# Kernel tuning notes

Measured on AMD Instinct MI355X. Metric: run time of the kernel, lower is better.

Reference implementation:

```python
import jax, jax.numpy as jnp
import numpy as np

N_NODES = 100000
N_EDGES = 1600000
IN_DIM, HID_DIM, OUT_DIM = 128, 128, 64


def setup_inputs() -> dict:
    key = jax.random.key(0)
    k1, k2, k3, k4 = jax.random.split(key, 4)
    x = jax.random.normal(k1, (N_NODES, IN_DIM), dtype=jnp.float32)
    edge_index = jax.random.randint(k2, (2, N_EDGES), 0, N_NODES, dtype=jnp.int64)
    # Glorot-ish init for weights, zeros for biases (as in PyG GCNConv defaults)
    W1 = jax.random.normal(k3, (IN_DIM, HID_DIM), dtype=jnp.float32) * (1.0 / np.sqrt(IN_DIM))
    b1 = jnp.zeros((HID_DIM,), dtype=jnp.float32)
    W2 = jax.random.normal(k4, (HID_DIM, OUT_DIM), dtype=jnp.float32) * (1.0 / np.sqrt(HID_DIM))
    b2 = jnp.zeros((OUT_DIM,), dtype=jnp.float32)
    return {"x": x, "edge_index": edge_index, "W1": W1, "b1": b1, "W2": W2, "b2": b2}


def _build_norm(edge_index, num_nodes):
    """Add self-loops and compute symmetric GCN normalization per edge.
    Returns (src, dst, norm) with self-loops appended."""
    loops = jnp.arange(num_nodes, dtype=edge_index.dtype)
    src = jnp.concatenate([edge_index[0], loops])
    dst = jnpp_concat = jnp.concatenate([edge_index[1], loops])
    deg = jax.ops.segment_sum(jnp.ones_like(dst, dtype=jnp.float32), dst,
                              num_segments=num_nodes)
    dinv = jax.lax.rsqrt(deg)  # deg >= 1 due to self-loops
    norm = dinv[src] * dinv[dst]  # [E + N]
    return src, dst, norm


def _gcn_conv(h, W, b, src, dst, norm, num_nodes):
    h = h @ W                                   # [N, F_out]
    msg = h[src] * norm[:, None]                # gather + scale, [E+N, F_out]
    agg = jax.ops.segment_sum(msg, dst, num_segments=num_nodes)
    return agg + b


def reference(x, edge_index, W1, b1, W2, b2):
    num_nodes = x.shape[0]
    src, dst, norm = _build_norm(edge_index, num_nodes)
    h = jax.nn.relu(_gcn_conv(x, W1, b1, src, dst, norm, num_nodes))
    return _gcn_conv(h, W2, b2, src, dst, norm, num_nodes)
```

## Files before the change

### kernel.cpp

```cpp
#include <hip/hip_runtime.h>

#define NN 100000
#define NE 1600000
#define NB 782
#define NBPAD 1024
#define CAPB 3072
#define EPB 8192
#define BFT 1024
#define NROWPAD 100096
#define DPAD 136
#define OPAD 72
#define MAXE 64

typedef __attribute__((ext_vector_type(8))) short short8;
typedef __attribute__((ext_vector_type(4))) float f32x4;

__device__ __forceinline__ unsigned short bf16rn(float f) {
    unsigned u = __float_as_uint(f);
    return (unsigned short)((u + 0x7FFFu + ((u >> 16) & 1u)) >> 16);
}
__device__ __forceinline__ float4 bf2x4(uint2 g) {
    float4 r;
    r.x = __uint_as_float(g.x << 16);
    r.y = __uint_as_float(g.x & 0xFFFF0000u);
    r.z = __uint_as_float(g.y << 16);
    r.w = __uint_as_float(g.y & 0xFFFF0000u);
    return r;
}
__device__ __forceinline__ uint2 packbf4(float4 v) {
    uint2 u;
    u.x = (unsigned)bf16rn(v.x) | ((unsigned)bf16rn(v.y) << 16);
    u.y = (unsigned)bf16rn(v.z) | ((unsigned)bf16rn(v.w) << 16);
    return u;
}
__device__ __forceinline__ void acc4(float4& a, uint2 v, float q) {
    a.x = fmaf(__uint_as_float(v.x << 16), q, a.x);
    a.y = fmaf(__uint_as_float(v.x & 0xFFFF0000u), q, a.y);
    a.z = fmaf(__uint_as_float(v.y << 16), q, a.z);
    a.w = fmaf(__uint_as_float(v.y & 0xFFFF0000u), q, a.w);
}
__device__ __forceinline__ float decq(unsigned e) {
    return __uint_as_float(0x38000000u | ((e & 0x7FFFu) << 12));
}
__device__ __forceinline__ int xcd_swz(int bid, int nwg) {
    int q = nwg >> 3, r = nwg & 7;
    int x = bid & 7, j = bid >> 3;
    int base = (x < r) ? x * (q + 1) : r * (q + 1) + (x - r) * q;
    return base + j;
}

__global__ void detect_i64_k(const unsigned* __restrict__ ei, int* __restrict__ flag) {
    unsigned w = ei[2 * threadIdx.x + 1];
    unsigned long long b = __ballot(w == 0u);
    if (threadIdx.x == 0) *flag = (b == 0xFFFFFFFFFFFFFFFFull) ? 1 : 0;
}
__device__ __forceinline__ int load_node(const void* ei, int i64, long long idx) {
    return i64 ? (int)((const long long*)ei)[idx] : ((const int*)ei)[idx];
}

__global__ void cast_bf16_k(const float* __restrict__ in, ushort* __restrict__ outb,
                            long long n4) {
    long long i = (long long)blockIdx.x * 256 + threadIdx.x;
    if (i >= n4) return;
    ((uint2*)outb)[i] = packbf4(((const float4*)in)[i]);
}

__global__ void prep_wt_k(const float* __restrict__ W1, const float* __restrict__ W2,
                          ushort* __restrict__ W1t, ushort* __restrict__ W2t) {
    int i = blockIdx.x * 256 + threadIdx.x;
    if (i < 128 * 128) {
        int k = i >> 7, n = i & 127;
        W1t[n * 128 + k] = bf16rn(W1[k * 128 + n]);
    }
    if (i < 128 * 64) {
        int k = i >> 6, n = i & 63;
        W2t[n * 128 + k] = bf16rn(W2[k * 64 + n]);
    }
}

__global__ __launch_bounds__(1024) void binfill_k(const void* __restrict__ ei,
                                                  const int* __restrict__ flag,
                                                  int* __restrict__ cur,
                                                  unsigned* __restrict__ bstage) {
    __shared__ unsigned binned[EPB];
    __shared__ int lcnt[NBPAD];
    __shared__ int lpos[NBPAD];
    __shared__ int gbase[NBPAD];
    __shared__ int tsum[NBPAD];
    int tid = threadIdx.x;
    long long e0 = (long long)blockIdx.x * EPB;
    int i64 = *flag;

    lcnt[tid] = 0;
    __syncthreads();

    for (int i = tid; i < EPB; i += BFT) {
        long long e = e0 + i;
        if (e < NE) {
            int d = load_node(ei, i64, (long long)NE + e);
            atomicAdd(&lcnt[d >> 7], 1);
        }
    }
    __syncthreads();

    int c = lcnt[tid];
    tsum[tid] = c;
    __syncthreads();
    for (int off = 1; off < NBPAD; off <<= 1) {
        int v = (tid >= off) ? tsum[tid - off] : 0;
        __syncthreads();
        tsum[tid] += v;
        __syncthreads();
    }
    int excl = tsum[tid] - c;
    lcnt[tid] = excl;
    lpos[tid] = excl;
    if (tid < NB) gbase[tid] = c ? atomicAdd(&cur[tid], c) : 0;
    __syncthreads();

    for (int i = tid; i < EPB; i += BFT) {
        long long e = e0 + i;
        if (e < NE) {
            int sv = load_node(ei, i64, e);
            int d  = load_node(ei, i64, (long long)NE + e);
            int b  = d >> 7;
            int p  = atomicAdd(&lpos[b], 1);
            binned[p] = ((unsigned)(d & 127) << 17) | (unsigned)sv;
        }
    }
    __syncthreads();

    if (tid < NB) {
        int start = lcnt[tid], endp = lpos[tid];
        int gb = gbase[tid];
        unsigned* dst = bstage + (long long)tid * CAPB;
        for (int k = start; k < endp; k++) {
            int go = gb + (k - start);
            if (go < CAPB) dst[go] = binned[k];
        }
    }
}

__global__ __launch_bounds__(256) void regroup_k(const int* __restrict__ cur,
                                                 const unsigned* __restrict__ bstage,
                                                 int* __restrict__ cnt,
                                                 int* __restrict__ rowstart,
                                                 unsigned* __restrict__ grouped,
                                                 float* __restrict__ dinv) {
    __shared__ unsigned stash[CAPB];
    __shared__ unsigned srt[CAPB];
    __shared__ int lcnt[128], lofs[128], lpos[128], sc[128];
    int tid = threadIdx.x;
    int b = blockIdx.x;

    int total = cur[b];
    if (total > CAPB) total = CAPB;
    const unsigned* seg = bstage + (long long)b * CAPB;
    for (int i = tid; i < total; i += 256) stash[i] = seg[i];
    __syncthreads();

    if (tid < 128) { lcnt[tid] = 0; lpos[tid] = 0; }
    __syncthreads();
    for (int i = tid; i < total; i += 256)
        atomicAdd(&lcnt[stash[i] >> 17], 1);
    __syncthreads();

    if (tid < 128) sc[tid] = lcnt[tid];
    __syncthreads();
    for (int off = 1; off < 128; off <<= 1) {
        int v = 0;
        if (tid < 128 && tid >= off) v = sc[tid - off];
        __syncthreads();
        if (tid < 128) sc[tid] += v;
        __syncthreads();
    }
    if (tid < 128) {
        lofs[tid] = sc[tid] - lcnt[tid];
        int node = b * 128 + tid;
        if (node < NN) {
            cnt[node] = lcnt[tid];
            rowstart[node] = b * CAPB + lofs[tid];
            dinv[node] = rsqrtf((float)(lcnt[tid] + 1));
        }
    }
    __syncthreads();

    for (int i = tid; i < total; i += 256) {
        unsigned e = stash[i];
        int nl = e >> 17;
        int p = atomicAdd(&lpos[nl], 1);
        srt[lofs[nl] + p] = e;
    }
    __syncthreads();

    unsigned* g = grouped + (long long)b * CAPB;
    for (int i = tid; i < total; i += 256) g[i] = srt[i] & 0x1FFFFu;
}

__global__ __launch_bounds__(256) void qn2_k(const int* __restrict__ cur,
                                             const float* __restrict__ dinv,
                                             unsigned* __restrict__ grouped) {
    int b = blockIdx.x;
    int total = cur[b];
    if (total > CAPB) total = CAPB;
    unsigned* g = grouped + (long long)b * CAPB;
    for (int i = threadIdx.x; i < total; i += 256) {
        unsigned s = g[i];
        unsigned bits = __float_as_uint(dinv[s]);
        g[i] = (s << 15) | ((bits >> 12) & 0x7FFFu);
    }
}

template <int LPN, bool BIAS, bool OUTB>
__global__ __launch_bounds__(256) void pull6_k(const unsigned* __restrict__ grouped,
                                               const int* __restrict__ rowstart,
                                               const int* __restrict__ cnt,
                                               const float* __restrict__ dinv,
                                               const ushort* __restrict__ hb,
                                               const float* __restrict__ bias,
                                               void* __restrict__ out) {
    __shared__ unsigned ed[256 / LPN][MAXE];
    int tid = threadIdx.x;
    int nib = tid / LPN;
    int lane = tid & (LPN - 1);
    int node = xcd_swz(blockIdx.x, (int)gridDim.x) * (256 / LPN) + nib;
    if (node >= NN) return;

    const uint2* h2 = (const uint2*)hb;
    float di = dinv[node];
    float w0 = di * di;
    float4 A = make_float4(0.f, 0.f, 0.f, 0.f);
    float4 B = make_float4(0.f, 0.f, 0.f, 0.f);
    {
        float4 hv = bf2x4(h2[(unsigned)node * LPN + lane]);
        A.x = hv.x * w0; A.y = hv.y * w0; A.z = hv.z * w0; A.w = hv.w * w0;
    }

    int deg = cnt[node];
    const unsigned* row = grouped + rowstart[node];
    int s = deg < MAXE ? deg : MAXE;

    for (int t = lane; t < s; t += LPN) ed[nib][t] = row[t];

    int j = 0;
    if (s >= 8) {
        uint2 v[8];
        float q[8];
#pragma unroll
        for (int t = 0; t < 8; t++) {
            unsigned e = ed[nib][t];
            q[t] = decq(e) * di;
            v[t] = h2[(e >> 15) * LPN + lane];
        }
        for (; j + 16 <= s; j += 8) {
#pragma unroll
            for (int t = 0; t < 8; t++) {
                unsigned e = ed[nib][j + 8 + t];
                uint2 nv = h2[(e >> 15) * LPN + lane];
                if (t & 1) acc4(B, v[t], q[t]);
                else       acc4(A, v[t], q[t]);
                v[t] = nv; q[t] = decq(e) * di;
            }
        }
#pragma unroll
        for (int t = 0; t < 8; t++) {
            if (t & 1) acc4(B, v[t], q[t]);
            else       acc4(A, v[t], q[t]);
        }
        j += 8;
    }
    for (; j < s; j++) {
        unsigned e = ed[nib][j];
        uint2 v0 = h2[(e >> 15) * LPN + lane];
        acc4(A, v0, decq(e) * di);
    }
    for (; j < deg; j++) {
        unsigned e = row[j];
        uint2 v0 = h2[(e >> 15) * LPN + lane];
        acc4(A, v0, decq(e) * di);
    }

    float4 o;
    o.x = A.x + B.x; o.y = A.y + B.y; o.z = A.z + B.z; o.w = A.w + B.w;
    if (BIAS) {
        float4 bb = ((const float4*)bias)[lane];
        o.x += bb.x; o.y += bb.y; o.z += bb.z; o.w += bb.w;
    }
    if (OUTB)
        ((uint2*)out)[(unsigned)node * LPN + lane] = packbf4(o);
    else
        ((float4*)out)[(unsigned)node * LPN + lane] = o;
}

__global__ __launch_bounds__(256) void dgemm_mfma_k(const ushort* __restrict__ Ab,
                                                    const ushort* __restrict__ W1t,
                                                    const float* __restrict__ b1,
                                                    const ushort* __restrict__ W2t,
                                                    ushort* __restrict__ H2b) {
    __shared__ ushort Tt[4][32 * DPAD];
    __shared__ ushort Ot[4][32 * OPAD];
    int tid = threadIdx.x;
    int wv = tid >> 6, lane = tid & 63;
    int m16 = lane & 15, quad = lane >> 4;
    int row0 = blockIdx.x * 128 + wv * 32;

    short8 af[2][4];
#pragma unroll
    for (int mt = 0; mt < 2; mt++)
#pragma unroll
        for (int kc = 0; kc < 4; kc++)
            af[mt][kc] = *(const short8*)(Ab + (long long)(row0 + mt * 16 + m16) * 128
                                          + kc * 32 + quad * 8);
    f32x4 accA[2][8];
#pragma unroll
    for (int mt = 0; mt < 2; mt++)
#pragma unroll
        for (int nt = 0; nt < 8; nt++) accA[mt][nt] = (f32x4){0.f, 0.f, 0.f, 0.f};

#pragma unroll
    for (int nt = 0; nt < 8; nt++) {
#pragma unroll
        for (int kc = 0; kc < 4; kc++) {
            short8 bf = *(const short8*)(W1t + (nt * 16 + m16) * 128 + kc * 32 + quad * 8);
            accA[0][nt] = __builtin_amdgcn_mfma_f32_16x16x32_bf16(af[0][kc], bf, accA[0][nt], 0, 0, 0);
            accA[1][nt] = __builtin_amdgcn_mfma_f32_16x16x32_bf16(af[1][kc], bf, accA[1][nt], 0, 0, 0);
        }
    }

#pragma unroll
    for (int nt = 0; nt < 8; nt++) {
        float bb = b1[nt * 16 + m16];
#pragma unroll
        for (int mt = 0; mt < 2; mt++)
#pragma unroll
            for (int r = 0; r < 4; r++) {
                float v = fmaxf(accA[mt][nt][r] + bb, 0.f);
                Tt[wv][(mt * 16 + quad * 4 + r) * DPAD + nt * 16 + m16] = bf16rn(v);
            }
    }
    __syncthreads();

    f32x4 accB[2][4];
#pragma unroll
    for (int mt = 0; mt < 2; mt++)
#pragma unroll
        for (int nt = 0; nt < 4; nt++) accB[mt][nt] = (f32x4){0.f, 0.f, 0.f, 0.f};

#pragma unroll
    for (int nt = 0; nt < 4; nt++) {
#pragma unroll
        for (int kc = 0; kc < 4; kc++) {
            short8 bf = *(const short8*)(W2t + (nt * 16 + m16) * 128 + kc * 32 + quad * 8);
#pragma unroll
            for (int mt = 0; mt < 2; mt++) {
                short8 aT = *(const short8*)(&Tt[wv][(mt * 16 + m16) * DPAD + kc * 32 + quad * 8]);
                accB[mt][nt] = __builtin_amdgcn_mfma_f32_16x16x32_bf16(aT, bf, accB[mt][nt], 0, 0, 0);
            }
        }
    }

#pragma unroll
    for (int nt = 0; nt < 4; nt++)
#pragma unroll
        for (int mt = 0; mt < 2; mt++)
#pragma unroll
            for (int r = 0; r < 4; r++)
                Ot[wv][(mt * 16 + quad * 4 + r) * OPAD + nt * 16 + m16] = bf16rn(accB[mt][nt][r]);
    __syncthreads();

    uint4* H4 = (uint4*)H2b;
#pragma unroll
    for (int it = 0; it < 4; it++) {
        int idx = it * 64 + lane;
        int r = idx >> 3, c = idx & 7;
        int grow = row0 + r;
        if (grow < NN) {
            uint4 v = *(const uint4*)(&Ot[wv][r * OPAD + c * 8]);
            H4[(long long)grow * 8 + c] = v;
        }
    }
}

extern "C" void kernel_launch(void* const* d_in, const int* in_sizes, int n_in,
                              void* d_out, int out_size, void* d_ws, size_t ws_size,
                              hipStream_t stream) {
    const float* x  = (const float*)d_in[0];
    const void*  ei = d_in[1];
    const float* W1 = (const float*)d_in[2];
    const float* b1 = (const float*)d_in[3];
    const float* W2 = (const float*)d_in[4];
    const float* b2 = (const float*)d_in[5];
    float* out = (float*)d_out;
    char* ws = (char*)d_ws;

    int*      flag     = (int*)ws;
    int*      cur      = (int*)(ws + 0x1000);
    int*      cnt      = (int*)(ws + 0x10000);
    int*      rowstart = (int*)(ws + 0x80000);
    unsigned* bstage   = (unsigned*)(ws + 0x100000);
    unsigned* grouped  = (unsigned*)(ws + 0xB00000);
    ushort*   xb       = (ushort*)(ws + 0x1500000);
    ushort*   aggxb    = (ushort*)(ws + 0x2F00000);
    ushort*   h2b      = (ushort*)(ws + 0x4800000);
    ushort*   W1t      = (ushort*)(ws + 0x5500000);
    ushort*   W2t      = (ushort*)(ws + 0x5510000);
    float*    dinv     = (float*)(ws + 0x5520000);

    hipMemsetAsync(cur, 0, NB * sizeof(int), stream);
    detect_i64_k<<<1, 64, 0, stream>>>((const unsigned*)ei, flag);
    cast_bf16_k<<<(NN * 32 + 255) / 256, 256, 0, stream>>>(x, xb, (long long)NN * 32);
    prep_wt_k<<<64, 256, 0, stream>>>(W1, W2, W1t, W2t);
    binfill_k<<<(NE + EPB - 1) / EPB, BFT, 0, stream>>>(ei, flag, cur, bstage);
    regroup_k<<<NB, 256, 0, stream>>>(cur, bstage, cnt, rowstart, grouped, dinv);
    qn2_k<<<NB, 256, 0, stream>>>(cur, dinv, grouped);

    pull6_k<32, false, true><<<(NN + 7) / 8, 256, 0, stream>>>(grouped, rowstart, cnt, dinv,
                                                               xb, nullptr, aggxb);
    dgemm_mfma_k<<<NROWPAD / 128, 256, 0, stream>>>(aggxb, W1t, b1, W2t, h2b);

    pull6_k<16, true, false><<<(NN + 15) / 16, 256, 0, stream>>>(grouped, rowstart, cnt, dinv,
                                                                 h2b, b2, out);
}
```

Before: 278.1 us.

## Split feature tables into column chunks and block-stage edge lists in LDS

The feature tables (bf16 x and layer-2 hidden) are re-laid out into column-chunk-major slabs of 16 features per node. Each pull block handles 64 nodes for a single chunk, with blockIdx low bits choosing the chunk. The intent is that the gathered working set per chunk is small enough to stay in L2/MALL cache. Each block stages the whole contiguous edge range of its 64 nodes into shared memory, replacing the per-node MAXE cap and tail path, and outputs use nontemporal stores. In exchange, the edge list is read NCH times, each gather is only 8 bytes, and a block's edge range larger than CAPB would overflow shared memory.

```diff
diff --git a/kernel.cpp b/kernel.cpp
--- a/kernel.cpp
+++ b/kernel.cpp
@@ -7,25 +7,18 @@
 #define CAPB 3072
 #define EPB 8192
 #define BFT 1024
+#define NPB 1563
 #define NROWPAD 100096
 #define DPAD 136
 #define OPAD 72
-#define MAXE 64
 
 typedef __attribute__((ext_vector_type(8))) short short8;
 typedef __attribute__((ext_vector_type(4))) float f32x4;
+typedef __attribute__((ext_vector_type(2))) unsigned u32x2;
 
 __device__ __forceinline__ unsigned short bf16rn(float f) {
     unsigned u = __float_as_uint(f);
     return (unsigned short)((u + 0x7FFFu + ((u >> 16) & 1u)) >> 16);
-}
-__device__ __forceinline__ float4 bf2x4(uint2 g) {
-    float4 r;
-    r.x = __uint_as_float(g.x << 16);
-    r.y = __uint_as_float(g.x & 0xFFFF0000u);
-    r.z = __uint_as_float(g.y << 16);
-    r.w = __uint_as_float(g.y & 0xFFFF0000u);
-    return r;
 }
 __device__ __forceinline__ uint2 packbf4(float4 v) {
     uint2 u;
@@ -42,12 +35,6 @@
 __device__ __forceinline__ float decq(unsigned e) {
     return __uint_as_float(0x38000000u | ((e & 0x7FFFu) << 12));
 }
-__device__ __forceinline__ int xcd_swz(int bid, int nwg) {
-    int q = nwg >> 3, r = nwg & 7;
-    int x = bid & 7, j = bid >> 3;
-    int base = (x < r) ? x * (q + 1) : r * (q + 1) + (x - r) * q;
-    return base + j;
-}
 
 __global__ void detect_i64_k(const unsigned* __restrict__ ei, int* __restrict__ flag) {
     unsigned w = ei[2 * threadIdx.x + 1];
@@ -58,11 +45,14 @@
     return i64 ? (int)((const long long*)ei)[idx] : ((const int*)ei)[idx];
 }
 
-__global__ void cast_bf16_k(const float* __restrict__ in, ushort* __restrict__ outb,
-                            long long n4) {
+__global__ void cast_xc_k(const float* __restrict__ in, ushort* __restrict__ xc) {
     long long i = (long long)blockIdx.x * 256 + threadIdx.x;
-    if (i >= n4) return;
-    ((uint2*)outb)[i] = packbf4(((const float4*)in)[i]);
+    if (i >= (long long)NN * 32) return;
+    int node = (int)(i >> 5);
+    int fq = (int)(i & 31);
+    int ch = fq >> 2, ln = fq & 3;
+    ((uint2*)xc)[(long long)ch * (NN * 4) + (long long)node * 4 + ln] =
+        packbf4(((const float4*)in)[i]);
 }
 
 __global__ void prep_wt_k(const float* __restrict__ W1, const float* __restrict__ W2,
@@ -211,52 +201,60 @@
     }
 }
 
-template <int LPN, bool BIAS, bool OUTB>
-__global__ __launch_bounds__(256) void pull6_k(const unsigned* __restrict__ grouped,
+template <int NCH, bool BIAS, bool OUTB>
+__global__ __launch_bounds__(256) void pull7_k(const unsigned* __restrict__ grouped,
                                                const int* __restrict__ rowstart,
                                                const int* __restrict__ cnt,
                                                const float* __restrict__ dinv,
-                                               const ushort* __restrict__ hb,
+                                               const ushort* __restrict__ tbl,
                                                const float* __restrict__ bias,
-                                               void* __restrict__ out) {
-    __shared__ unsigned ed[256 / LPN][MAXE];
+                                               void* __restrict__ outp) {
+    __shared__ unsigned eds[CAPB];
     int tid = threadIdx.x;
-    int nib = tid / LPN;
-    int lane = tid & (LPN - 1);
-    int node = xcd_swz(blockIdx.x, (int)gridDim.x) * (256 / LPN) + nib;
+    int bid = blockIdx.x;
+    int c  = bid & (NCH - 1);
+    int nb = bid / NCH;
+    int node0 = nb * 64;
+
+    int nlast = node0 + 63; if (nlast >= NN) nlast = NN - 1;
+    int base = rowstart[node0];
+    int size = rowstart[nlast] + cnt[nlast] - base;
+    for (int i = tid; i < size; i += 256)
+        eds[i] = __builtin_nontemporal_load(&grouped[base + i]);
+
+    int node = node0 + (tid >> 2);
+    int lane = tid & 3;
+    __syncthreads();
     if (node >= NN) return;
 
-    const uint2* h2 = (const uint2*)hb;
+    const uint2* tc = (const uint2*)tbl + (long long)c * (NN * 4);
     float di = dinv[node];
     float w0 = di * di;
     float4 A = make_float4(0.f, 0.f, 0.f, 0.f);
     float4 B = make_float4(0.f, 0.f, 0.f, 0.f);
     {
-        float4 hv = bf2x4(h2[(unsigned)node * LPN + lane]);
-        A.x = hv.x * w0; A.y = hv.y * w0; A.z = hv.z * w0; A.w = hv.w * w0;
+        uint2 sv = tc[(unsigned)node * 4 + lane];
+        acc4(A, sv, w0);
     }
 
     int deg = cnt[node];
-    const unsigned* row = grouped + rowstart[node];
-    int s = deg < MAXE ? deg : MAXE;
-
-    for (int t = lane; t < s; t += LPN) ed[nib][t] = row[t];
+    int off = rowstart[node] - base;
 
     int j = 0;
-    if (s >= 8) {
+    if (deg >= 8) {
         uint2 v[8];
         float q[8];
 #pragma unroll
         for (int t = 0; t < 8; t++) {
-            unsigned e = ed[nib][t];
+            unsigned e = eds[off + t];
             q[t] = decq(e) * di;
-            v[t] = h2[(e >> 15) * LPN + lane];
-        }
-        for (; j + 16 <= s; j += 8) {
+            v[t] = tc[(e >> 15) * 4 + lane];
+        }
+        for (; j + 16 <= deg; j += 8) {
 #pragma unroll
             for (int t = 0; t < 8; t++) {
-                unsigned e = ed[nib][j + 8 + t];
-                uint2 nv = h2[(e >> 15) * LPN + lane];
+                unsigned e = eds[off + j + 8 + t];
+                uint2 nv = tc[(e >> 15) * 4 + lane];
                 if (t & 1) acc4(B, v[t], q[t]);
                 else       acc4(A, v[t], q[t]);
                 v[t] = nv; q[t] = decq(e) * di;
@@ -269,27 +267,28 @@
         }
         j += 8;
     }
-    for (; j < s; j++) {
-        unsigned e = ed[nib][j];
-        uint2 v0 = h2[(e >> 15) * LPN + lane];
-        acc4(A, v0, decq(e) * di);
-    }
     for (; j < deg; j++) {
-        unsigned e = row[j];
-        uint2 v0 = h2[(e >> 15) * LPN + lane];
+        unsigned e = eds[off + j];
+        uint2 v0 = tc[(e >> 15) * 4 + lane];
         acc4(A, v0, decq(e) * di);
     }
 
     float4 o;
     o.x = A.x + B.x; o.y = A.y + B.y; o.z = A.z + B.z; o.w = A.w + B.w;
     if (BIAS) {
-        float4 bb = ((const float4*)bias)[lane];
+        float4 bb = ((const float4*)bias)[c * 4 + lane];
         o.x += bb.x; o.y += bb.y; o.z += bb.z; o.w += bb.w;
     }
-    if (OUTB)
-        ((uint2*)out)[(unsigned)node * LPN + lane] = packbf4(o);
-    else
-        ((float4*)out)[(unsigned)node * LPN + lane] = o;
+    if (OUTB) {
+        uint2 p = packbf4(o);
+        u32x2 pv; pv.x = p.x; pv.y = p.y;
+        __builtin_nontemporal_store(pv,
+            (u32x2*)&((uint2*)outp)[(long long)node * 32 + c * 4 + lane]);
+    } else {
+        f32x4 ov; ov.x = o.x; ov.y = o.y; ov.z = o.z; ov.w = o.w;
+        __builtin_nontemporal_store(ov,
+            (f32x4*)&((float4*)outp)[(long long)node * 16 + c * 4 + lane]);
+    }
 }
 
 __global__ __launch_bounds__(256) void dgemm_mfma_k(const ushort* __restrict__ Ab,
@@ -372,11 +371,11 @@
 #pragma unroll
     for (int it = 0; it < 4; it++) {
         int idx = it * 64 + lane;
-        int r = idx >> 3, c = idx & 7;
+        int r = idx >> 3, cc = idx & 7;
         int grow = row0 + r;
         if (grow < NN) {
-            uint4 v = *(const uint4*)(&Ot[wv][r * OPAD + c * 8]);
-            H4[(long long)grow * 8 + c] = v;
+            uint4 v = *(const uint4*)(&Ot[wv][r * OPAD + cc * 8]);
+            H4[(long long)(cc >> 1) * (NN * 2) + (long long)grow * 2 + (cc & 1)] = v;
         }
     }
 }
@@ -399,25 +398,25 @@
     int*      rowstart = (int*)(ws + 0x80000);
     unsigned* bstage   = (unsigned*)(ws + 0x100000);
     unsigned* grouped  = (unsigned*)(ws + 0xB00000);
-    ushort*   xb       = (ushort*)(ws + 0x1500000);
+    ushort*   xc       = (ushort*)(ws + 0x1500000);
     ushort*   aggxb    = (ushort*)(ws + 0x2F00000);
-    ushort*   h2b      = (ushort*)(ws + 0x4800000);
+    ushort*   h2c      = (ushort*)(ws + 0x4800000);
     ushort*   W1t      = (ushort*)(ws + 0x5500000);
     ushort*   W2t      = (ushort*)(ws + 0x5510000);
     float*    dinv     = (float*)(ws + 0x5520000);
 
     hipMemsetAsync(cur, 0, NB * sizeof(int), stream);
     detect_i64_k<<<1, 64, 0, stream>>>((const unsigned*)ei, flag);
-    cast_bf16_k<<<(NN * 32 + 255) / 256, 256, 0, stream>>>(x, xb, (long long)NN * 32);
+    cast_xc_k<<<(NN * 32 + 255) / 256, 256, 0, stream>>>(x, xc);
     prep_wt_k<<<64, 256, 0, stream>>>(W1, W2, W1t, W2t);
     binfill_k<<<(NE + EPB - 1) / EPB, BFT, 0, stream>>>(ei, flag, cur, bstage);
     regroup_k<<<NB, 256, 0, stream>>>(cur, bstage, cnt, rowstart, grouped, dinv);
     qn2_k<<<NB, 256, 0, stream>>>(cur, dinv, grouped);
 
-    pull6_k<32, false, true><<<(NN + 7) / 8, 256, 0, stream>>>(grouped, rowstart, cnt, dinv,
-                                                               xb, nullptr, aggxb);
-    dgemm_mfma_k<<<NROWPAD / 128, 256, 0, stream>>>(aggxb, W1t, b1, W2t, h2b);
-
-    pull6_k<16, true, false><<<(NN + 15) / 16, 256, 0, stream>>>(grouped, rowstart, cnt, dinv,
-                                                                 h2b, b2, out);
-}
+    pull7_k<8, false, true><<<8 * NPB, 256, 0, stream>>>(grouped, rowstart, cnt, dinv,
+                                                         xc, nullptr, aggxb);
+    dgemm_mfma_k<<<NROWPAD / 128, 256, 0, stream>>>(aggxb, W1t, b1, W2t, h2c);
+
+    pull7_k<4, true, false><<<4 * NPB, 256, 0, stream>>>(grouped, rowstart, cnt, dinv,
+                                                         h2c, b2, out);
+}
```

New measurement: 340.9 us. +22.6%, slower.
